# Optimization experiments

Hardware: AMD Instinct MI355X
Metric: run time of the kernel (lower is better)

## Reference

```python
import jax, jax.numpy as jnp
import numpy as np

EMBED = 1024
HEADS = 16
HEAD_DIM = EMBED // HEADS


def setup_inputs() -> dict:
    key = jax.random.key(0)
    ks = jax.random.split(key, 7)
    s = 1.0 / np.sqrt(EMBED)
    return {
        "hidden_states": jax.random.normal(ks[0], (8, 1024, EMBED), dtype=jnp.float32),
        "w_q": jax.random.uniform(ks[1], (EMBED, EMBED), jnp.float32, -s, s),
        "b_q": jax.random.uniform(ks[2], (EMBED,), jnp.float32, -s, s),
        "w_k": jax.random.uniform(ks[3], (EMBED, EMBED), jnp.float32, -s, s),
        "b_k": jax.random.uniform(ks[4], (EMBED,), jnp.float32, -s, s),
        "w_v": jax.random.uniform(ks[5], (EMBED, EMBED), jnp.float32, -s, s),
        "b_v": jax.random.uniform(ks[6], (EMBED,), jnp.float32, -s, s),
    }


def reference(hidden_states, w_q, b_q, w_k, b_k, w_v, b_v):
    b, L, c = hidden_states.shape
    h, d = HEADS, HEAD_DIM
    # torch Linear: x @ W.T + b
    q = hidden_states @ w_q.T + b_q
    k = hidden_states @ w_k.T + b_k
    v = hidden_states @ w_v.T + b_v
    # [b, L, h, d] -> [b, h, L, d]
    q = q.reshape(b, L, h, d).transpose(0, 2, 1, 3)
    k = k.reshape(b, L, h, d).transpose(0, 2, 1, 3)
    v = v.reshape(b, L, h, d).transpose(0, 2, 1, 3)
    scores = jnp.einsum("bhqd,bhkd->bhqk", q, k) * (d ** -0.5)
    probs = jax.nn.softmax(scores, axis=-1)
    out = jnp.einsum("bhqk,bhkd->bhqd", probs, v)  # [b, h, L, d]
    # Faithful to original: .view(b, L, -1) on [b,h,L,d] WITHOUT head transpose
    return out.reshape(b, L, h * d)
```

## Files before the change

### kernel.cpp

```cpp
#include <hip/hip_runtime.h>

#define EMBED 1024
#define HEADS 16
#define HDIM  64

typedef __attribute__((ext_vector_type(8))) short bf16x8;
typedef __attribute__((ext_vector_type(8))) _Float16 f16x8;
typedef __attribute__((ext_vector_type(4))) float f32x4;

#define AS1 __attribute__((address_space(1)))
#define AS3 __attribute__((address_space(3)))

#if __has_builtin(__builtin_amdgcn_exp2f)
#define EXP2F(x) __builtin_amdgcn_exp2f(x)
#else
#define EXP2F(x) exp2f(x)
#endif

__device__ __forceinline__ unsigned bf16_rne(float f) {
    unsigned u = __float_as_uint(f);
    return (u + 0x7FFFu + ((u >> 16) & 1u)) >> 16;
}

__global__ __launch_bounds__(256)
void cast_all(const float* __restrict__ X,  const float* __restrict__ Wq,
              const float* __restrict__ Wk, const float* __restrict__ Wv,
              short* __restrict__ Xh, short* __restrict__ Wh)
{
    const int bid = blockIdx.x;
    const float* in;
    short* out;
    float scale;
    int base;
    if (bid < 4096) { in = X; out = Xh; scale = 1.0f; base = bid; }
    else {
        const int wsel = (bid - 4096) >> 9;
        in  = (wsel == 0) ? Wq : (wsel == 1) ? Wk : Wv;
        out = Wh + wsel * 1048576;
        scale = 256.0f;
        base = (bid - 4096) & 511;
    }
    const int i = (base * 256 + threadIdx.x) * 8;
    float4 a = *(const float4*)(in + i);
    float4 b = *(const float4*)(in + i + 4);
    float f[8] = {a.x, a.y, a.z, a.w, b.x, b.y, b.z, b.w};
    union { _Float16 h[8]; uint4 v; } H;
#pragma unroll
    for (int e = 0; e < 8; ++e) H.h[e] = (_Float16)(f[e] * scale);
    *(uint4*)(out + i) = H.v;
}

#define STAGE_A(buf, h, kt) do {                                              \
    const short* s0_ = baseA + ((h) * 128) * EMBED + (kt) * 64;               \
    short* d_ = &sh[(buf) * 32768 + (h) * 8192 + t * 8];                      \
    __builtin_amdgcn_global_load_lds((const AS1 void*)s0_, (AS3 void*)d_, 16, 0, 0); \
    __builtin_amdgcn_global_load_lds((const AS1 void*)(s0_ + 64 * EMBED), (AS3 void*)(d_ + 4096), 16, 0, 0); \
} while (0)

#define STAGE_B(buf, h, kt) do {                                              \
    const short* s0_ = baseB + ((h) * 32) * EMBED + (kt) * 64;                \
    short* d_ = &sh[(buf) * 32768 + 16384 + (h) * 8192 + t * 8];              \
    __builtin_amdgcn_global_load_lds((const AS1 void*)s0_, (AS3 void*)d_, 16, 0, 0); \
    __builtin_amdgcn_global_load_lds((const AS1 void*)(s0_ + 128 * EMBED), (AS3 void*)(d_ + 4096), 16, 0, 0); \
} while (0)

__global__ __launch_bounds__(512, 2)
void qkv_mfma(const short* __restrict__ Xh, const short* __restrict__ Wh,
              const float* __restrict__ bq, const float* __restrict__ bk,
              const float* __restrict__ bv,
              short* __restrict__ Qb, short* __restrict__ Kb, short* __restrict__ Vn)
{
    __shared__ short sh[65536];

    const int t = threadIdx.x;
    const int lane = t & 63, quad = lane >> 4, l16 = lane & 15;
    const int w = t >> 6, wm = w >> 2, wn = w & 3;

    const int n0 = blockIdx.x * 256;
    const int m0 = blockIdx.y * 256;

    const int r  = t >> 3;
    const int k8 = ((t & 7) ^ (r & 7)) * 8;
    const short* baseA = Xh + (size_t)(m0 + r) * EMBED + k8;
    const short* baseB = Wh + (size_t)(n0 + (r & 31) + (r >> 5) * 64) * EMBED + k8;

    const int xk0 = ((quad * 16)      ^ ((l16 & 7) << 4)) >> 1;
    const int xk1 = ((64 + quad * 16) ^ ((l16 & 7) << 4)) >> 1;
    const int aOff = wm * 8192 + l16 * 64;
    const int bOff = 16384 + wn * 2048 + l16 * 64;

    f32x4 acc[8][4];
#pragma unroll
    for (int i = 0; i < 8; ++i)
#pragma unroll
        for (int j = 0; j < 4; ++j) acc[i][j] = (f32x4){0.f, 0.f, 0.f, 0.f};

    STAGE_B(0, 0, 0);
    STAGE_A(0, 0, 0);
    STAGE_A(0, 1, 0);
    STAGE_B(0, 1, 0);
    asm volatile("s_waitcnt vmcnt(4)" ::: "memory");
    __builtin_amdgcn_s_barrier();

#pragma unroll 1
    for (int i = 0; i < 8; ++i) {
        const int ktb = 2 * i + 1;
        const int ktc = 2 * i + 2;
        const bool more = (i < 7);
#pragma unroll
        for (int p = 0; p < 8; ++p) {
            const int q = p & 3, buf = p >> 2;
            const int miH = (q & 1) * 4, niH = (q >> 1) * 2;

            f16x8 af[4][2], bf[2][2];
#pragma unroll
            for (int mi = 0; mi < 4; ++mi) {
                const int o = buf * 32768 + aOff + (miH + mi) * 1024;
                af[mi][0] = *(const f16x8*)&sh[o + xk0];
                af[mi][1] = *(const f16x8*)&sh[o + xk1];
            }
#pragma unroll
            for (int ni = 0; ni < 2; ++ni) {
                const int nig = niH + ni;
                const int o = buf * 32768 + bOff + (nig & 1) * 1024 + (nig >> 1) * 8192;
                bf[ni][0] = *(const f16x8*)&sh[o + xk0];
                bf[ni][1] = *(const f16x8*)&sh[o + xk1];
            }

            if      (p == 0) STAGE_B(1, 0, ktb);
            else if (p == 1) STAGE_A(1, 0, ktb);
            else if (p == 2) STAGE_A(1, 1, ktb);
            else if (p == 3) STAGE_B(1, 1, ktb);
            else if (more) {
                if      (p == 4) STAGE_B(0, 0, ktc);
                else if (p == 5) STAGE_A(0, 0, ktc);
                else if (p == 6) STAGE_A(0, 1, ktc);
                else             STAGE_B(0, 1, ktc);
            }

            if (p < 4 || more) asm volatile("s_waitcnt vmcnt(4)" ::: "memory");
            else if (p == 4)   asm volatile("s_waitcnt vmcnt(0)" ::: "memory");
            else               asm volatile("" ::: "memory");
            __builtin_amdgcn_s_barrier();

            __builtin_amdgcn_s_setprio(1);
#pragma unroll
            for (int mi = 0; mi < 4; ++mi)
#pragma unroll
                for (int ni = 0; ni < 2; ++ni) {
                    acc[miH + mi][niH + ni] = __builtin_amdgcn_mfma_f32_16x16x32_f16(
                        af[mi][0], bf[ni][0], acc[miH + mi][niH + ni], 0, 0, 0);
                    acc[miH + mi][niH + ni] = __builtin_amdgcn_mfma_f32_16x16x32_f16(
                        af[mi][1], bf[ni][1], acc[miH + mi][niH + ni], 0, 0, 0);
                }
            __builtin_amdgcn_s_setprio(0);
            __builtin_amdgcn_s_barrier();
        }
    }

    const int mat = n0 >> 10;
    const float* bias = (mat == 0) ? bq : (mat == 1) ? bk : bv;
    short* Out = (mat == 0) ? Qb : (mat == 1) ? Kb : Vn;
    const float s = (mat == 0) ? 0.125f * 1.4426950408889634f : 1.0f;
    const float fs = s * (1.0f / 256.0f);
    const int nm0 = n0 & 1023;
    float bias_v[4];
#pragma unroll
    for (int ni = 0; ni < 4; ++ni) bias_v[ni] = bias[nm0 + wn * 64 + ni * 16 + l16] * s;
    const int bidx = m0 >> 10;
    const int l0   = m0 & 1023;

#pragma unroll
    for (int mi = 0; mi < 8; ++mi) {
        __syncthreads();
#pragma unroll
        for (int ni = 0; ni < 4; ++ni) {
            const int col = wn * 64 + ni * 16 + l16;
#pragma unroll
            for (int rr = 0; rr < 4; ++rr) {
                const int srow = wm * 16 + quad * 4 + rr;
                sh[srow * 268 + col] =
                    (short)(unsigned short)bf16_rne(fmaf(acc[mi][ni][rr], fs, bias_v[ni]));
            }
        }
        __syncthreads();
        const int srw = t >> 4;
        const int c0  = (t & 15) * 16;
        uint4 v0 = *(uint4*)&sh[srw * 268 + c0];
        uint4 v1 = *(uint4*)&sh[srw * 268 + c0 + 8];
        const int wmS = srw >> 4, rloc = srw & 15;
        const int l = l0 + wmS * 128 + mi * 16 + rloc;
        const int nm = nm0 + c0;
        const int head = nm >> 6, d0 = nm & 63;
        short* pDst = Out + ((size_t)(bidx * HEADS + head) * 1024 + l) * 64 + d0;
        *(uint4*)pDst = v0;
        *(uint4*)(pDst + 8) = v1;
    }
}

__global__ __launch_bounds__(256)
void vtrans(const short* __restrict__ Vn, short* __restrict__ Vt)
{
    __shared__ int tile[64 * 65];
    const int t  = threadIdx.x;
    const int lt = blockIdx.x;
    const int bh = blockIdx.y;
    const int lq = t >> 3, dc = (t & 7) * 8;
    const short* src = Vn + ((size_t)bh * 1024 + lt * 64) * 64;
#pragma unroll
    for (int h = 0; h < 2; ++h) {
        const int l = lq + h * 32;
        union { uint4 v; unsigned short us[8]; } ld;
        ld.v = *(const uint4*)&src[l * 64 + dc];
#pragma unroll
        for (int j = 0; j < 8; ++j) tile[(dc + j) * 65 + l] = ld.us[j];
    }
    __syncthreads();
    const int dr = t >> 3, lblk = (t & 7) * 8;
    short* dst = Vt + (size_t)bh * 64 * 1024 + lt * 64;
#pragma unroll
    for (int h = 0; h < 2; ++h) {
        const int d = dr + h * 32;
        union { uint4 v; unsigned short us[8]; } o;
#pragma unroll
        for (int j = 0; j < 8; ++j) o.us[j] = (unsigned short)tile[d * 65 + lblk + j];
        *(uint4*)&dst[(size_t)d * 1024 + lblk] = o.v;
    }
}

__global__ __launch_bounds__(256)
void attn_mfma(const short* __restrict__ Qb, const short* __restrict__ Kb,
               const short* __restrict__ Vt, float* __restrict__ out)
{
    __shared__ short smem[20480];

    const int t  = threadIdx.x;
    const int id  = blockIdx.x;
    const int xcd = id & 7;
    const int loc = id >> 3;
    const int bh  = xcd * 16 + (loc >> 4);
    const int qt  = loc & 15;
    const int lane = t & 63, quad = lane >> 4, l16 = lane & 15;
    const int w = t >> 6;
    const int srow = t & 63, schunk = t >> 6;

    const int prow = ((srow >> 4) & 1) * 32 + ((srow >> 2) & 3) * 8
                   + (srow >> 5) * 4 + (srow & 3);

    {
        const short* gq = Qb + ((size_t)bh * 1024 + qt * 64 + srow) * 64 + schunk * 8;
        __builtin_amdgcn_global_load_lds((const AS1 void*)gq,        (AS3 void*)&smem[t * 8],         16, 0, 0);
        __builtin_amdgcn_global_load_lds((const AS1 void*)(gq + 32), (AS3 void*)&smem[(t + 256) * 8], 16, 0, 0);
        const short* gk = Kb + ((size_t)bh * 1024 + prow) * 64 + schunk * 8;
        __builtin_amdgcn_global_load_lds((const AS1 void*)gk,        (AS3 void*)&smem[4096 + t * 8],         16, 0, 0);
        __builtin_amdgcn_global_load_lds((const AS1 void*)(gk + 32), (AS3 void*)&smem[4096 + (t + 256) * 8], 16, 0, 0);
        const short* gv = Vt + ((size_t)bh * 64 + srow) * 1024 + schunk * 8;
        __builtin_amdgcn_global_load_lds((const AS1 void*)gv,        (AS3 void*)&smem[12288 + t * 8],         16, 0, 0);
        __builtin_amdgcn_global_load_lds((const AS1 void*)(gv + 32), (AS3 void*)&smem[12288 + (t + 256) * 8], 16, 0, 0);
    }
    __syncthreads();

    bf16x8 qfrag[2];
#pragma unroll
    for (int kh = 0; kh < 2; ++kh)
        qfrag[kh] = *(const bf16x8*)&smem[((quad + 4 * kh) * 64 + w * 16 + l16) * 8];

    f32x4 O[4];
#pragma unroll
    for (int i = 0; i < 4; ++i) O[i] = (f32x4){0.f, 0.f, 0.f, 0.f};
    float l_i = 0.f;

    for (int kt = 0; kt < 16; ++kt) {
        const int cur = kt & 1, nxt = cur ^ 1;
        if (kt < 15) {
            const short* gk = Kb + ((size_t)bh * 1024 + (kt + 1) * 64 + prow) * 64 + schunk * 8;
            __builtin_amdgcn_global_load_lds((const AS1 void*)gk,        (AS3 void*)&smem[4096 + nxt * 4096 + t * 8],         16, 0, 0);
            __builtin_amdgcn_global_load_lds((const AS1 void*)(gk + 32), (AS3 void*)&smem[4096 + nxt * 4096 + (t + 256) * 8], 16, 0, 0);
            const short* gv = Vt + ((size_t)bh * 64 + srow) * 1024 + (kt + 1) * 64 + schunk * 8;
            __builtin_amdgcn_global_load_lds((const AS1 void*)gv,        (AS3 void*)&smem[12288 + nxt * 4096 + t * 8],         16, 0, 0);
            __builtin_amdgcn_global_load_lds((const AS1 void*)(gv + 32), (AS3 void*)&smem[12288 + nxt * 4096 + (t + 256) * 8], 16, 0, 0);
        }

        const short* Kc = &smem[4096 + cur * 4096];
        const short* Vc = &smem[12288 + cur * 4096];

        f32x4 ST[4];
#pragma unroll
        for (int mi = 0; mi < 4; ++mi) ST[mi] = (f32x4){0.f, 0.f, 0.f, 0.f};
        __builtin_amdgcn_s_setprio(1);
#pragma unroll
        for (int kh = 0; kh < 2; ++kh)
#pragma unroll
            for (int mi = 0; mi < 4; ++mi) {
                const bf16x8 ka = *(const bf16x8*)&Kc[((quad + 4 * kh) * 64 + mi * 16 + l16) * 8];
                ST[mi] = __builtin_amdgcn_mfma_f32_16x16x32_bf16(ka, qfrag[kh], ST[mi], 0, 0, 0);
            }
        __builtin_amdgcn_s_setprio(0);

        float p[4][4];
        float rs = 0.f;
#pragma unroll
        for (int mi = 0; mi < 4; ++mi)
#pragma unroll
            for (int rr = 0; rr < 4; ++rr) { p[mi][rr] = EXP2F(ST[mi][rr]); rs += p[mi][rr]; }
        l_i += rs;

        union { unsigned u[4]; bf16x8 v; } pa[2];
#pragma unroll
        for (int kh = 0; kh < 2; ++kh) {
            asm("v_cvt_pk_bf16_f32 %0, %1, %2" : "=v"(pa[kh].u[0]) : "v"(p[kh][0]),     "v"(p[kh][1]));
            asm("v_cvt_pk_bf16_f32 %0, %1, %2" : "=v"(pa[kh].u[1]) : "v"(p[kh][2]),     "v"(p[kh][3]));
            asm("v_cvt_pk_bf16_f32 %0, %1, %2" : "=v"(pa[kh].u[2]) : "v"(p[kh + 2][0]), "v"(p[kh + 2][1]));
            asm("v_cvt_pk_bf16_f32 %0, %1, %2" : "=v"(pa[kh].u[3]) : "v"(p[kh + 2][2]), "v"(p[kh + 2][3]));
        }

        __builtin_amdgcn_s_setprio(1);
#pragma unroll
        for (int kh = 0; kh < 2; ++kh)
#pragma unroll
            for (int mi = 0; mi < 4; ++mi) {
                const bf16x8 va = *(const bf16x8*)&Vc[((quad + 4 * kh) * 64 + mi * 16 + l16) * 8];
                O[mi] = __builtin_amdgcn_mfma_f32_16x16x32_bf16(va, pa[kh].v, O[mi], 0, 0, 0);
            }
        __builtin_amdgcn_s_setprio(0);

        __syncthreads();
    }

    l_i += __shfl_xor(l_i, 16);
    l_i += __shfl_xor(l_i, 32);

    float* Os = (float*)&smem[4096];
    const float inv = 1.0f / l_i;
#pragma unroll
    for (int mi = 0; mi < 4; ++mi) {
        f32x4 v;
#pragma unroll
        for (int rr = 0; rr < 4; ++rr) v[rr] = O[mi][rr] * inv;
        *(f32x4*)&Os[(w * 16 + l16) * 68 + mi * 16 + quad * 4] = v;
    }
    __syncthreads();
    {
        const int q = t >> 2, dbase = (t & 3) * 16;
        float* op = out + ((size_t)bh * 1024 + qt * 64 + q) * 64 + dbase;
#pragma unroll
        for (int i = 0; i < 4; ++i)
            *(float4*)&op[i * 4] = *(float4*)&Os[q * 68 + dbase + i * 4];
    }
}

extern "C" void kernel_launch(void* const* d_in, const int* in_sizes, int n_in,
                              void* d_out, int out_size, void* d_ws, size_t ws_size,
                              hipStream_t stream)
{
    const float* X  = (const float*)d_in[0];
    const float* Wq = (const float*)d_in[1];
    const float* bq = (const float*)d_in[2];
    const float* Wk = (const float*)d_in[3];
    const float* bk = (const float*)d_in[4];
    const float* Wv = (const float*)d_in[5];
    const float* bv = (const float*)d_in[6];
    float* out = (float*)d_out;

    const size_t per = (size_t)8 * HEADS * 1024 * HDIM;
    short* Qb = (short*)d_ws;
    short* Kb = Qb + per;
    short* Vt = Kb + per;
    short* Xh = Vt + per;
    short* Wh = Xh + per;
    short* Vn = (short*)d_out;

    cast_all<<<4096 + 3 * 512, 256, 0, stream>>>(X, Wq, Wk, Wv, Xh, Wh);

    qkv_mfma<<<dim3(12, 32), 512, 0, stream>>>(Xh, Wh, bq, bk, bv, Qb, Kb, Vn);
    vtrans<<<dim3(16, 128), 256, 0, stream>>>(Vn, Vt);
    attn_mfma<<<2048, 256, 0, stream>>>(Qb, Kb, Vt, out);
}
```

Baseline: 242.4 us.

## Shrink QKV GEMM tile to 256x128, triple-buffer LDS, XCD-aware block mapping

The QKV projection GEMM tile drops from 256x256 to 256x128 per block, and the launch goes from 384 to 768 blocks on a 1D grid. Block IDs are remapped so that blocks landing on the same XCD share N columns, which should improve L2 reuse. The k-loop moves from double to triple buffering in LDS with a deeper prefetch distance and a looser vmcnt wait, so that loads overlap compute better. In exchange, the smaller tile lowers arithmetic intensity per block and raises LDS use to 144KB per block, which may limit occupancy to one block per CU despite launch_bounds(512,2).

Measured after the change: 254.4 us. 4.9% more time.

```diff
diff --git a/kernel.cpp b/kernel.cpp
--- a/kernel.cpp
+++ b/kernel.cpp
@@ -52,16 +52,16 @@
 
 #define STAGE_A(buf, h, kt) do {                                              \
     const short* s0_ = baseA + ((h) * 128) * EMBED + (kt) * 64;               \
-    short* d_ = &sh[(buf) * 32768 + (h) * 8192 + t * 8];                      \
+    short* d_ = &sh[(buf) * 24576 + (h) * 8192 + t * 8];                      \
     __builtin_amdgcn_global_load_lds((const AS1 void*)s0_, (AS3 void*)d_, 16, 0, 0); \
     __builtin_amdgcn_global_load_lds((const AS1 void*)(s0_ + 64 * EMBED), (AS3 void*)(d_ + 4096), 16, 0, 0); \
 } while (0)
 
-#define STAGE_B(buf, h, kt) do {                                              \
-    const short* s0_ = baseB + ((h) * 32) * EMBED + (kt) * 64;                \
-    short* d_ = &sh[(buf) * 32768 + 16384 + (h) * 8192 + t * 8];              \
+#define STAGE_B(buf, kt) do {                                                 \
+    const short* s0_ = baseB + (kt) * 64;                                     \
+    short* d_ = &sh[(buf) * 24576 + 16384 + t * 8];                           \
     __builtin_amdgcn_global_load_lds((const AS1 void*)s0_, (AS3 void*)d_, 16, 0, 0); \
-    __builtin_amdgcn_global_load_lds((const AS1 void*)(s0_ + 128 * EMBED), (AS3 void*)(d_ + 4096), 16, 0, 0); \
+    __builtin_amdgcn_global_load_lds((const AS1 void*)(s0_ + 64 * EMBED), (AS3 void*)(d_ + 4096), 16, 0, 0); \
 } while (0)
 
 __global__ __launch_bounds__(512, 2)
@@ -70,82 +70,83 @@
               const float* __restrict__ bv,
               short* __restrict__ Qb, short* __restrict__ Kb, short* __restrict__ Vn)
 {
-    __shared__ short sh[65536];
+    __shared__ short sh[73728];
 
     const int t = threadIdx.x;
     const int lane = t & 63, quad = lane >> 4, l16 = lane & 15;
-    const int w = t >> 6, wm = w >> 2, wn = w & 3;
-
-    const int n0 = blockIdx.x * 256;
-    const int m0 = blockIdx.y * 256;
+    const int w = t >> 6, wm = w >> 1, wn = w & 1;
+
+    const int id  = blockIdx.x;
+    const int xcd = id & 7, loc = id >> 3;
+    const int bx  = xcd * 3 + (loc >> 5);
+    const int by  = loc & 31;
+    const int n0 = bx * 128, m0 = by * 256;
 
     const int r  = t >> 3;
     const int k8 = ((t & 7) ^ (r & 7)) * 8;
     const short* baseA = Xh + (size_t)(m0 + r) * EMBED + k8;
-    const short* baseB = Wh + (size_t)(n0 + (r & 31) + (r >> 5) * 64) * EMBED + k8;
+    const short* baseB = Wh + (size_t)(n0 + r) * EMBED + k8;
 
     const int xk0 = ((quad * 16)      ^ ((l16 & 7) << 4)) >> 1;
     const int xk1 = ((64 + quad * 16) ^ ((l16 & 7) << 4)) >> 1;
-    const int aOff = wm * 8192 + l16 * 64;
-    const int bOff = 16384 + wn * 2048 + l16 * 64;
-
-    f32x4 acc[8][4];
-#pragma unroll
-    for (int i = 0; i < 8; ++i)
+    const int aBase = (wm >> 1) * 8192 + ((wm & 1) * 64 + l16) * 64;
+    const int bBase = 16384 + (wn * 64 + l16) * 64;
+
+    f32x4 acc[4][4];
+#pragma unroll
+    for (int i = 0; i < 4; ++i)
 #pragma unroll
         for (int j = 0; j < 4; ++j) acc[i][j] = (f32x4){0.f, 0.f, 0.f, 0.f};
 
-    STAGE_B(0, 0, 0);
-    STAGE_A(0, 0, 0);
-    STAGE_A(0, 1, 0);
-    STAGE_B(0, 1, 0);
-    asm volatile("s_waitcnt vmcnt(4)" ::: "memory");
+    STAGE_A(0, 0, 0); STAGE_A(0, 1, 0); STAGE_B(0, 0);
+    STAGE_A(1, 0, 1); STAGE_A(1, 1, 1); STAGE_B(1, 1);
+    asm volatile("s_waitcnt vmcnt(0)" ::: "memory");
     __builtin_amdgcn_s_barrier();
 
+    int bufE = 0;
 #pragma unroll 1
     for (int i = 0; i < 8; ++i) {
-        const int ktb = 2 * i + 1;
-        const int ktc = 2 * i + 2;
+        const int bufO  = (bufE + 1 == 3) ? 0 : bufE + 1;
+        const int bufS1 = (bufO + 1 == 3) ? 0 : bufO + 1;
+        const int ktc = 2 * i + 2, ktd = 2 * i + 3;
         const bool more = (i < 7);
+        const int obE = bufE * 24576, obO = bufO * 24576;
 #pragma unroll
         for (int p = 0; p < 8; ++p) {
-            const int q = p & 3, buf = p >> 2;
-            const int miH = (q & 1) * 4, niH = (q >> 1) * 2;
-
-            f16x8 af[4][2], bf[2][2];
-#pragma unroll
-            for (int mi = 0; mi < 4; ++mi) {
-                const int o = buf * 32768 + aOff + (miH + mi) * 1024;
+            const int q = p & 3;
+            const int ob = (p < 4) ? obE : obO;
+            const int miH = (q & 1) * 2, niH = (q >> 1) * 2;
+
+            f16x8 af[2][2], bf[2][2];
+#pragma unroll
+            for (int mi = 0; mi < 2; ++mi) {
+                const int o = ob + aBase + (miH + mi) * 1024;
                 af[mi][0] = *(const f16x8*)&sh[o + xk0];
                 af[mi][1] = *(const f16x8*)&sh[o + xk1];
             }
 #pragma unroll
             for (int ni = 0; ni < 2; ++ni) {
-                const int nig = niH + ni;
-                const int o = buf * 32768 + bOff + (nig & 1) * 1024 + (nig >> 1) * 8192;
+                const int o = ob + bBase + (niH + ni) * 1024;
                 bf[ni][0] = *(const f16x8*)&sh[o + xk0];
                 bf[ni][1] = *(const f16x8*)&sh[o + xk1];
             }
 
-            if      (p == 0) STAGE_B(1, 0, ktb);
-            else if (p == 1) STAGE_A(1, 0, ktb);
-            else if (p == 2) STAGE_A(1, 1, ktb);
-            else if (p == 3) STAGE_B(1, 1, ktb);
-            else if (more) {
-                if      (p == 4) STAGE_B(0, 0, ktc);
-                else if (p == 5) STAGE_A(0, 0, ktc);
-                else if (p == 6) STAGE_A(0, 1, ktc);
-                else             STAGE_B(0, 1, ktc);
-            }
-
-            if (p < 4 || more) asm volatile("s_waitcnt vmcnt(4)" ::: "memory");
-            else if (p == 4)   asm volatile("s_waitcnt vmcnt(0)" ::: "memory");
-            else               asm volatile("" ::: "memory");
+            if (more) {
+                if      (p == 0) STAGE_A(bufS1, 0, ktc);
+                else if (p == 1) STAGE_A(bufS1, 1, ktc);
+                else if (p == 2) STAGE_B(bufS1, ktc);
+                else if (p == 4) STAGE_A(bufE, 0, ktd);
+                else if (p == 5) STAGE_A(bufE, 1, ktd);
+                else if (p == 6) STAGE_B(bufE, ktd);
+            }
+
+            if (more) asm volatile("s_waitcnt vmcnt(2)" ::: "memory");
+            else      asm volatile("s_waitcnt vmcnt(0)" ::: "memory");
             __builtin_amdgcn_s_barrier();
 
             __builtin_amdgcn_s_setprio(1);
 #pragma unroll
-            for (int mi = 0; mi < 4; ++mi)
+            for (int mi = 0; mi < 2; ++mi)
 #pragma unroll
                 for (int ni = 0; ni < 2; ++ni) {
                     acc[miH + mi][niH + ni] = __builtin_amdgcn_mfma_f32_16x16x32_f16(
@@ -156,6 +157,7 @@
             __builtin_amdgcn_s_setprio(0);
             __builtin_amdgcn_s_barrier();
         }
+        bufE = bufS1;
     }
 
     const int mat = n0 >> 10;
@@ -171,7 +173,7 @@
     const int l0   = m0 & 1023;
 
 #pragma unroll
-    for (int mi = 0; mi < 8; ++mi) {
+    for (int mi = 0; mi < 4; ++mi) {
         __syncthreads();
 #pragma unroll
         for (int ni = 0; ni < 4; ++ni) {
@@ -179,18 +181,18 @@
 #pragma unroll
             for (int rr = 0; rr < 4; ++rr) {
                 const int srow = wm * 16 + quad * 4 + rr;
-                sh[srow * 268 + col] =
+                sh[srow * 132 + col] =
                     (short)(unsigned short)bf16_rne(fmaf(acc[mi][ni][rr], fs, bias_v[ni]));
             }
         }
         __syncthreads();
-        const int srw = t >> 4;
-        const int c0  = (t & 15) * 16;
-        uint4 v0 = *(uint4*)&sh[srw * 268 + c0];
-        uint4 v1 = *(uint4*)&sh[srw * 268 + c0 + 8];
-        const int wmS = srw >> 4, rloc = srw & 15;
-        const int l = l0 + wmS * 128 + mi * 16 + rloc;
-        const int nm = nm0 + c0;
+        const int srowR = t >> 3;
+        const int cblk  = (t & 7) * 16;
+        uint4 v0 = *(uint4*)&sh[srowR * 132 + cblk];
+        uint4 v1 = *(uint4*)&sh[srowR * 132 + cblk + 8];
+        const int wmS = srowR >> 4, rloc = srowR & 15;
+        const int l = l0 + wmS * 64 + mi * 16 + rloc;
+        const int nm = nm0 + cblk;
         const int head = nm >> 6, d0 = nm & 63;
         short* pDst = Out + ((size_t)(bidx * HEADS + head) * 1024 + l) * 64 + d0;
         *(uint4*)pDst = v0;
@@ -372,7 +374,7 @@
 
     cast_all<<<4096 + 3 * 512, 256, 0, stream>>>(X, Wq, Wk, Wv, Xh, Wh);
 
-    qkv_mfma<<<dim3(12, 32), 512, 0, stream>>>(Xh, Wh, bq, bk, bv, Qb, Kb, Vn);
+    qkv_mfma<<<768, 512, 0, stream>>>(Xh, Wh, bq, bk, bv, Qb, Kb, Vn);
     vtrans<<<dim3(16, 128), 256, 0, stream>>>(Vn, Vt);
     attn_mfma<<<2048, 256, 0, stream>>>(Qb, Kb, Vt, out);
 }
```

## Process two query tiles per attention block to reuse K/V tiles

Applied to the files above, without the earlier changes.

Each attention workgroup now handles 128 query rows (two 64-row subtiles) instead of 64, so every K and V tile loaded into LDS feeds twice the MFMA work. The grid is halved to 1024 blocks and the LDS layout is rearranged to hold both Q subtiles. This cuts global K/V traffic and per-block load overhead, in exchange for more registers, more LDS per block, and fewer blocks for latency hiding.

Measured after the change: 228.9 us. -5.6%, faster.

```diff
diff --git a/kernel.cpp b/kernel.cpp
--- a/kernel.cpp
+++ b/kernel.cpp
@@ -232,14 +232,14 @@
 void attn_mfma(const short* __restrict__ Qb, const short* __restrict__ Kb,
                const short* __restrict__ Vt, float* __restrict__ out)
 {
-    __shared__ short smem[20480];
+    __shared__ short smem[25088];
 
     const int t  = threadIdx.x;
     const int id  = blockIdx.x;
     const int xcd = id & 7;
     const int loc = id >> 3;
-    const int bh  = xcd * 16 + (loc >> 4);
-    const int qt  = loc & 15;
+    const int bh  = xcd * 16 + (loc >> 3);
+    const int qt  = loc & 7;
     const int lane = t & 63, quad = lane >> 4, l16 = lane & 15;
     const int w = t >> 6;
     const int srow = t & 63, schunk = t >> 6;
@@ -248,101 +248,116 @@
                    + (srow >> 5) * 4 + (srow & 3);
 
     {
-        const short* gq = Qb + ((size_t)bh * 1024 + qt * 64 + srow) * 64 + schunk * 8;
-        __builtin_amdgcn_global_load_lds((const AS1 void*)gq,        (AS3 void*)&smem[t * 8],         16, 0, 0);
-        __builtin_amdgcn_global_load_lds((const AS1 void*)(gq + 32), (AS3 void*)&smem[(t + 256) * 8], 16, 0, 0);
+#pragma unroll
+        for (int u = 0; u < 2; ++u) {
+            const short* gq = Qb + ((size_t)bh * 1024 + qt * 128 + u * 64 + srow) * 64 + schunk * 8;
+            __builtin_amdgcn_global_load_lds((const AS1 void*)gq,        (AS3 void*)&smem[16384 + u * 4096 + t * 8],         16, 0, 0);
+            __builtin_amdgcn_global_load_lds((const AS1 void*)(gq + 32), (AS3 void*)&smem[16384 + u * 4096 + (t + 256) * 8], 16, 0, 0);
+        }
         const short* gk = Kb + ((size_t)bh * 1024 + prow) * 64 + schunk * 8;
-        __builtin_amdgcn_global_load_lds((const AS1 void*)gk,        (AS3 void*)&smem[4096 + t * 8],         16, 0, 0);
-        __builtin_amdgcn_global_load_lds((const AS1 void*)(gk + 32), (AS3 void*)&smem[4096 + (t + 256) * 8], 16, 0, 0);
+        __builtin_amdgcn_global_load_lds((const AS1 void*)gk,        (AS3 void*)&smem[t * 8],         16, 0, 0);
+        __builtin_amdgcn_global_load_lds((const AS1 void*)(gk + 32), (AS3 void*)&smem[(t + 256) * 8], 16, 0, 0);
         const short* gv = Vt + ((size_t)bh * 64 + srow) * 1024 + schunk * 8;
-        __builtin_amdgcn_global_load_lds((const AS1 void*)gv,        (AS3 void*)&smem[12288 + t * 8],         16, 0, 0);
-        __builtin_amdgcn_global_load_lds((const AS1 void*)(gv + 32), (AS3 void*)&smem[12288 + (t + 256) * 8], 16, 0, 0);
+        __builtin_amdgcn_global_load_lds((const AS1 void*)gv,        (AS3 void*)&smem[8192 + t * 8],         16, 0, 0);
+        __builtin_amdgcn_global_load_lds((const AS1 void*)(gv + 32), (AS3 void*)&smem[8192 + (t + 256) * 8], 16, 0, 0);
     }
     __syncthreads();
 
-    bf16x8 qfrag[2];
-#pragma unroll
-    for (int kh = 0; kh < 2; ++kh)
-        qfrag[kh] = *(const bf16x8*)&smem[((quad + 4 * kh) * 64 + w * 16 + l16) * 8];
-
-    f32x4 O[4];
-#pragma unroll
-    for (int i = 0; i < 4; ++i) O[i] = (f32x4){0.f, 0.f, 0.f, 0.f};
-    float l_i = 0.f;
+    bf16x8 qfrag[2][2];
+#pragma unroll
+    for (int u = 0; u < 2; ++u)
+#pragma unroll
+        for (int kh = 0; kh < 2; ++kh)
+            qfrag[u][kh] = *(const bf16x8*)&smem[16384 + u * 4096 + ((quad + 4 * kh) * 64 + w * 16 + l16) * 8];
+
+    f32x4 O[2][4];
+#pragma unroll
+    for (int u = 0; u < 2; ++u)
+#pragma unroll
+        for (int i = 0; i < 4; ++i) O[u][i] = (f32x4){0.f, 0.f, 0.f, 0.f};
+    float l_i[2] = {0.f, 0.f};
 
     for (int kt = 0; kt < 16; ++kt) {
         const int cur = kt & 1, nxt = cur ^ 1;
         if (kt < 15) {
             const short* gk = Kb + ((size_t)bh * 1024 + (kt + 1) * 64 + prow) * 64 + schunk * 8;
-            __builtin_amdgcn_global_load_lds((const AS1 void*)gk,        (AS3 void*)&smem[4096 + nxt * 4096 + t * 8],         16, 0, 0);
-            __builtin_amdgcn_global_load_lds((const AS1 void*)(gk + 32), (AS3 void*)&smem[4096 + nxt * 4096 + (t + 256) * 8], 16, 0, 0);
+            __builtin_amdgcn_global_load_lds((const AS1 void*)gk,        (AS3 void*)&smem[nxt * 4096 + t * 8],         16, 0, 0);
+            __builtin_amdgcn_global_load_lds((const AS1 void*)(gk + 32), (AS3 void*)&smem[nxt * 4096 + (t + 256) * 8], 16, 0, 0);
             const short* gv = Vt + ((size_t)bh * 64 + srow) * 1024 + (kt + 1) * 64 + schunk * 8;
-            __builtin_amdgcn_global_load_lds((const AS1 void*)gv,        (AS3 void*)&smem[12288 + nxt * 4096 + t * 8],         16, 0, 0);
-            __builtin_amdgcn_global_load_lds((const AS1 void*)(gv + 32), (AS3 void*)&smem[12288 + nxt * 4096 + (t + 256) * 8], 16, 0, 0);
-        }
-
-        const short* Kc = &smem[4096 + cur * 4096];
-        const short* Vc = &smem[12288 + cur * 4096];
-
-        f32x4 ST[4];
-#pragma unroll
-        for (int mi = 0; mi < 4; ++mi) ST[mi] = (f32x4){0.f, 0.f, 0.f, 0.f};
-        __builtin_amdgcn_s_setprio(1);
-#pragma unroll
-        for (int kh = 0; kh < 2; ++kh)
-#pragma unroll
-            for (int mi = 0; mi < 4; ++mi) {
-                const bf16x8 ka = *(const bf16x8*)&Kc[((quad + 4 * kh) * 64 + mi * 16 + l16) * 8];
-                ST[mi] = __builtin_amdgcn_mfma_f32_16x16x32_bf16(ka, qfrag[kh], ST[mi], 0, 0, 0);
-            }
-        __builtin_amdgcn_s_setprio(0);
-
-        float p[4][4];
-        float rs = 0.f;
-#pragma unroll
-        for (int mi = 0; mi < 4; ++mi)
-#pragma unroll
-            for (int rr = 0; rr < 4; ++rr) { p[mi][rr] = EXP2F(ST[mi][rr]); rs += p[mi][rr]; }
-        l_i += rs;
-
-        union { unsigned u[4]; bf16x8 v; } pa[2];
-#pragma unroll
-        for (int kh = 0; kh < 2; ++kh) {
-            asm("v_cvt_pk_bf16_f32 %0, %1, %2" : "=v"(pa[kh].u[0]) : "v"(p[kh][0]),     "v"(p[kh][1]));
-            asm("v_cvt_pk_bf16_f32 %0, %1, %2" : "=v"(pa[kh].u[1]) : "v"(p[kh][2]),     "v"(p[kh][3]));
-            asm("v_cvt_pk_bf16_f32 %0, %1, %2" : "=v"(pa[kh].u[2]) : "v"(p[kh + 2][0]), "v"(p[kh + 2][1]));
-            asm("v_cvt_pk_bf16_f32 %0, %1, %2" : "=v"(pa[kh].u[3]) : "v"(p[kh + 2][2]), "v"(p[kh + 2][3]));
-        }
-
-        __builtin_amdgcn_s_setprio(1);
-#pragma unroll
-        for (int kh = 0; kh < 2; ++kh)
-#pragma unroll
-            for (int mi = 0; mi < 4; ++mi) {
-                const bf16x8 va = *(const bf16x8*)&Vc[((quad + 4 * kh) * 64 + mi * 16 + l16) * 8];
-                O[mi] = __builtin_amdgcn_mfma_f32_16x16x32_bf16(va, pa[kh].v, O[mi], 0, 0, 0);
-            }
-        __builtin_amdgcn_s_setprio(0);
-
-        __syncthreads();
-    }
-
-    l_i += __shfl_xor(l_i, 16);
-    l_i += __shfl_xor(l_i, 32);
-
-    float* Os = (float*)&smem[4096];
-    const float inv = 1.0f / l_i;
-#pragma unroll
-    for (int mi = 0; mi < 4; ++mi) {
-        f32x4 v;
-#pragma unroll
-        for (int rr = 0; rr < 4; ++rr) v[rr] = O[mi][rr] * inv;
-        *(f32x4*)&Os[(w * 16 + l16) * 68 + mi * 16 + quad * 4] = v;
-    }
-    __syncthreads();
-    {
+            __builtin_amdgcn_global_load_lds((const AS1 void*)gv,        (AS3 void*)&smem[8192 + nxt * 4096 + t * 8],         16, 0, 0);
+            __builtin_amdgcn_global_load_lds((const AS1 void*)(gv + 32), (AS3 void*)&smem[8192 + nxt * 4096 + (t + 256) * 8], 16, 0, 0);
+        }
+
+        const short* Kc = &smem[cur * 4096];
+        const short* Vc = &smem[8192 + cur * 4096];
+
+#pragma unroll
+        for (int u = 0; u < 2; ++u) {
+            f32x4 ST[4];
+#pragma unroll
+            for (int mi = 0; mi < 4; ++mi) ST[mi] = (f32x4){0.f, 0.f, 0.f, 0.f};
+            __builtin_amdgcn_s_setprio(1);
+#pragma unroll
+            for (int kh = 0; kh < 2; ++kh)
+#pragma unroll
+                for (int mi = 0; mi < 4; ++mi) {
+                    const bf16x8 ka = *(const bf16x8*)&Kc[((quad + 4 * kh) * 64 + mi * 16 + l16) * 8];
+                    ST[mi] = __builtin_amdgcn_mfma_f32_16x16x32_bf16(ka, qfrag[u][kh], ST[mi], 0, 0, 0);
+                }
+            __builtin_amdgcn_s_setprio(0);
+
+            float p[4][4];
+            float rs = 0.f;
+#pragma unroll
+            for (int mi = 0; mi < 4; ++mi)
+#pragma unroll
+                for (int rr = 0; rr < 4; ++rr) { p[mi][rr] = EXP2F(ST[mi][rr]); rs += p[mi][rr]; }
+            l_i[u] += rs;
+
+            union { unsigned uu[4]; bf16x8 v; } pa[2];
+#pragma unroll
+            for (int kh = 0; kh < 2; ++kh) {
+                asm("v_cvt_pk_bf16_f32 %0, %1, %2" : "=v"(pa[kh].uu[0]) : "v"(p[kh][0]),     "v"(p[kh][1]));
+                asm("v_cvt_pk_bf16_f32 %0, %1, %2" : "=v"(pa[kh].uu[1]) : "v"(p[kh][2]),     "v"(p[kh][3]));
+                asm("v_cvt_pk_bf16_f32 %0, %1, %2" : "=v"(pa[kh].uu[2]) : "v"(p[kh + 2][0]), "v"(p[kh + 2][1]));
+                asm("v_cvt_pk_bf16_f32 %0, %1, %2" : "=v"(pa[kh].uu[3]) : "v"(p[kh + 2][2]), "v"(p[kh + 2][3]));
+            }
+
+            __builtin_amdgcn_s_setprio(1);
+#pragma unroll
+            for (int kh = 0; kh < 2; ++kh)
+#pragma unroll
+                for (int mi = 0; mi < 4; ++mi) {
+                    const bf16x8 va = *(const bf16x8*)&Vc[((quad + 4 * kh) * 64 + mi * 16 + l16) * 8];
+                    O[u][mi] = __builtin_amdgcn_mfma_f32_16x16x32_bf16(va, pa[kh].v, O[u][mi], 0, 0, 0);
+                }
+            __builtin_amdgcn_s_setprio(0);
+        }
+
+        __syncthreads();
+    }
+
+#pragma unroll
+    for (int u = 0; u < 2; ++u) {
+        l_i[u] += __shfl_xor(l_i[u], 16);
+        l_i[u] += __shfl_xor(l_i[u], 32);
+    }
+
+    float* Os = (float*)&smem[16384];
+#pragma unroll
+    for (int u = 0; u < 2; ++u) {
+        __syncthreads();
+        const float inv = 1.0f / l_i[u];
+#pragma unroll
+        for (int mi = 0; mi < 4; ++mi) {
+            f32x4 v;
+#pragma unroll
+            for (int rr = 0; rr < 4; ++rr) v[rr] = O[u][mi][rr] * inv;
+            *(f32x4*)&Os[(w * 16 + l16) * 68 + mi * 16 + quad * 4] = v;
+        }
+        __syncthreads();
         const int q = t >> 2, dbase = (t & 3) * 16;
-        float* op = out + ((size_t)bh * 1024 + qt * 64 + q) * 64 + dbase;
+        float* op = out + ((size_t)bh * 1024 + qt * 128 + u * 64 + q) * 64 + dbase;
 #pragma unroll
         for (int i = 0; i < 4; ++i)
             *(float4*)&op[i * 4] = *(float4*)&Os[q * 68 + dbase + i * 4];
@@ -374,5 +389,5 @@
 
     qkv_mfma<<<dim3(12, 32), 512, 0, stream>>>(Xh, Wh, bq, bk, bv, Qb, Kb, Vn);
     vtrans<<<dim3(16, 128), 256, 0, stream>>>(Vn, Vt);
-    attn_mfma<<<2048, 256, 0, stream>>>(Qb, Kb, Vt, out);
-}
+    attn_mfma<<<1024, 256, 0, stream>>>(Qb, Kb, Vt, out);
+}
```
